# Optimization experiments

Hardware: AMD Instinct MI355X
Metric: run time of the kernel (lower is better)

The kernel has to match this reference:

```python
import jax, jax.numpy as jnp
import numpy as np
import math

DIM_EMB = 1024
DIM_QK = 1024
DIM_V = 1024
NORM_FACT = 1.0 / math.sqrt(DIM_EMB)

def setup_inputs() -> dict:
    key = jax.random.key(0)
    k0, k1, k2, k3 = jax.random.split(key, 4)
    x = jax.random.normal(k0, (4, 4096, DIM_EMB), dtype=jnp.float32)
    # nn.Linear weights are [out_features, in_features]; y = x @ W.T
    s = 1.0 / math.sqrt(DIM_EMB)
    Wq = jax.random.uniform(k1, (DIM_QK, DIM_EMB), jnp.float32, -s, s)
    Wk = jax.random.uniform(k2, (DIM_QK, DIM_EMB), jnp.float32, -s, s)
    Wv = jax.random.uniform(k3, (DIM_V, DIM_EMB), jnp.float32, -s, s)
    return {"x": x, "Wq": Wq, "Wk": Wk, "Wv": Wv}

def reference(x, Wq, Wk, Wv):
    # q,k,v: [b, n, d]
    q = jnp.einsum('bne,de->bnd', x, Wq)
    k = jnp.einsum('bne,de->bnd', x, Wk)
    v = jnp.einsum('bne,de->bnd', x, Wv)
    logits = jnp.einsum('bnd,bmd->bnm', q, k)  # [b, n, n]
    # Faithful to source: softmax over last dim FIRST, then scale by 1/sqrt(dim_embedding)
    score = jax.nn.softmax(logits, axis=-1) * NORM_FACT
    att = jnp.einsum('bnm,bmv->bnv', score, v)
    return att
```

## Files before the change

### kernel.cpp

```cpp
#include <hip/hip_runtime.h>
#include <hip/hip_bf16.h>

typedef _Float16 f16;
typedef _Float16 f16x4 __attribute__((ext_vector_type(4)));
typedef _Float16 f16x8 __attribute__((ext_vector_type(8)));
typedef float f32x4 __attribute__((ext_vector_type(4)));

__device__ __forceinline__ void gload16(const void* g, void* l) {
    __builtin_amdgcn_global_load_lds(
        (const __attribute__((address_space(1))) void*)g,
        (__attribute__((address_space(3))) void*)l, 16, 0, 0);
}

#define FENCE asm volatile("" ::: "memory")
#define BARRIER do { FENCE; __builtin_amdgcn_s_barrier(); FENCE; } while (0)

#define PHASE_MFMA(QI, QJ)                                                    \
    __builtin_amdgcn_s_setprio(1);                                            \
    _Pragma("unroll")                                                         \
    for (int ks = 0; ks < 2; ++ks)                                            \
      _Pragma("unroll")                                                       \
      for (int i = 0; i < 4; ++i)                                             \
        _Pragma("unroll")                                                     \
        for (int j = 0; j < 2; ++j)                                           \
          acc[(QI)*4 + i][(QJ)*2 + j] = __builtin_amdgcn_mfma_f32_16x16x32_f16( \
              a[i][ks], b[j][ks], acc[(QI)*4 + i][(QJ)*2 + j], 0, 0, 0);      \
    __builtin_amdgcn_s_setprio(0);

#define BT8_BODY(KBASE, NTILES)                                               \
    const int rr8 = lane >> 3;                                                \
    const int cs  = ((lane & 7) ^ rr8) << 3;                                  \
    const int ldsr = wid << 3;                                                \
    auto stageA = [&](int kt, int c, int h) {                                 \
        const size_t g0 = (size_t)(bm + (h << 7) + ldsr + rr8) * lda + (KBASE) + kt + cs; \
        gload16(A + g0,                      &sA[c][((h << 7) + ldsr) << 6]); \
        gload16(A + g0 + ((size_t)lda << 6), &sA[c][((h << 7) + 64 + ldsr) << 6]); \
    };                                                                        \
    auto stageB = [&](int kt, int c, int h) {                                 \
        const size_t g0 = (size_t)(bn + (h << 7) + ldsr + rr8) * ldb + (KBASE) + kt + cs; \
        gload16(B + g0,                      &sB[c][((h << 7) + ldsr) << 6]); \
        gload16(B + g0 + ((size_t)ldb << 6), &sB[c][((h << 7) + 64 + ldsr) << 6]); \
    };                                                                        \
    f32x4 acc[8][4] = {};                                                     \
    f16x8 a[4][2], b[2][2];                                                   \
    auto loadA = [&](int c, int qi) {                                         \
        _Pragma("unroll")                                                     \
        for (int i = 0; i < 4; ++i) {                                         \
            const int ra = wr * 128 + (qi * 4 + i) * 16 + (lane & 15);        \
            const int swz = (ra & 7) << 3;                                    \
            _Pragma("unroll")                                                 \
            for (int ks = 0; ks < 2; ++ks) {                                  \
                const int kk = ks * 32 + (lane >> 4) * 8;                     \
                a[i][ks] = *(const f16x8*)(&sA[c][(ra << 6) + (kk ^ swz)]);   \
            }                                                                 \
        }                                                                     \
    };                                                                        \
    auto loadB = [&](int c, int qj) {                                         \
        _Pragma("unroll")                                                     \
        for (int j = 0; j < 2; ++j) {                                         \
            const int rb = wc * 64 + (qj * 2 + j) * 16 + (lane & 15);         \
            const int swz = (rb & 7) << 3;                                    \
            _Pragma("unroll")                                                 \
            for (int ks = 0; ks < 2; ++ks) {                                  \
                const int kk = ks * 32 + (lane >> 4) * 8;                     \
                b[j][ks] = *(const f16x8*)(&sB[c][(rb << 6) + (kk ^ swz)]);   \
            }                                                                 \
        }                                                                     \
    };                                                                        \
    stageA(0, 0, 0); stageA(0, 0, 1); stageB(0, 0, 0); stageB(0, 0, 1);       \
    asm volatile("s_waitcnt vmcnt(0)" ::: "memory");                          \
    BARRIER;                                                                  \
    for (int g = 0; g < (NTILES); ++g) {                                      \
        const int c = g & 1, cn = c ^ 1;                                      \
        const int kn = (g + 1) << 6;                                          \
        const bool more = (g + 1) < (NTILES);                                 \
        loadA(c, 0); loadB(c, 0);                                             \
        if (more) { stageA(kn, cn, 0); stageA(kn, cn, 1); }                   \
        BARRIER; PHASE_MFMA(0, 0); BARRIER;                                   \
        loadB(c, 1);                                                          \
        if (more) { stageB(kn, cn, 0); stageB(kn, cn, 1); }                   \
        BARRIER; PHASE_MFMA(0, 1); BARRIER;                                   \
        loadA(c, 1); loadB(c, 0);                                             \
        BARRIER; PHASE_MFMA(1, 0); BARRIER;                                   \
        loadB(c, 1);                                                          \
        asm volatile("s_waitcnt vmcnt(0)" ::: "memory");                      \
        BARRIER; PHASE_MFMA(1, 1); BARRIER;                                   \
    }

template<bool F16OUT>
__global__ __launch_bounds__(512) void gemm_bt8(
    const f16* __restrict__ A, const f16* __restrict__ B, void* __restrict__ Cv,
    int K, int lda, int ldb, int ldc, float scale, int nbn)
{
    __shared__ f16 sA[2][256 * 64];
    __shared__ f16 sB[2][256 * 64];
    const int tid = threadIdx.x, lane = tid & 63, wid = tid >> 6;
    const int wr = wid >> 2, wc = wid & 3;
    const int cpx = gridDim.x >> 3;
    const int wg = (blockIdx.x & 7) * cpx + (blockIdx.x >> 3);
    const int bm = (wg / nbn) << 8, bn = (wg % nbn) << 8;

    BT8_BODY(0, K >> 6)

#pragma unroll
    for (int i = 0; i < 8; ++i)
#pragma unroll
        for (int j = 0; j < 4; ++j)
#pragma unroll
            for (int r = 0; r < 4; ++r) {
                const int row = bm + wr * 128 + i * 16 + ((lane >> 4) << 2) + r;
                const int col = bn + wc * 64 + j * 16 + (lane & 15);
                if constexpr (F16OUT)
                    ((f16*)Cv)[(size_t)row * ldc + col] = (f16)(acc[i][j][r] * scale);
                else
                    ((float*)Cv)[(size_t)row * ldc + col] = acc[i][j][r] * scale;
            }
}

__global__ __launch_bounds__(512) void gemm_qk(
    const f16* __restrict__ A, const f16* __restrict__ B,
    f16* __restrict__ P, float* __restrict__ mst, float* __restrict__ sst,
    int lda, int ldb)
{
    __shared__ f16 sA[2][256 * 64];
    __shared__ f16 sB[2][256 * 64];
    const int tid = threadIdx.x, lane = tid & 63, wid = tid >> 6;
    const int wr = wid >> 2, wc = wid & 3;
    const int cpx = gridDim.x >> 3;
    const int wg = (blockIdx.x & 7) * cpx + (blockIdx.x >> 3);
    const int bm = (wg >> 4) << 8, bn = (wg & 15) << 8;

    BT8_BODY(0, 16)

    float* red = (float*)sA;
    const int lg = lane >> 4;
#pragma unroll
    for (int i = 0; i < 8; ++i)
#pragma unroll
        for (int r = 0; r < 4; ++r) {
            float v = fmaxf(fmaxf(acc[i][0][r], acc[i][1][r]),
                            fmaxf(acc[i][2][r], acc[i][3][r]));
#pragma unroll
            for (int msk = 1; msk <= 8; msk <<= 1) v = fmaxf(v, __shfl_xor(v, msk));
            if ((lane & 15) == 0) red[wr * 512 + (i * 16 + lg * 4 + r) * 4 + wc] = v;
        }
    BARRIER;
    float mloc[8][4];
#pragma unroll
    for (int i = 0; i < 8; ++i)
#pragma unroll
        for (int r = 0; r < 4; ++r) {
            const float4 q = *(const float4*)&red[wr * 512 + (i * 16 + lg * 4 + r) * 4];
            mloc[i][r] = fmaxf(fmaxf(q.x, q.y), fmaxf(q.z, q.w));
        }
    BARRIER;
#pragma unroll
    for (int i = 0; i < 8; ++i)
#pragma unroll
        for (int r = 0; r < 4; ++r) {
            float s = 0.f;
#pragma unroll
            for (int j = 0; j < 4; ++j) {
                const float e = __expf(acc[i][j][r] - mloc[i][r]);
                acc[i][j][r] = e; s += e;
            }
#pragma unroll
            for (int msk = 1; msk <= 8; msk <<= 1) s += __shfl_xor(s, msk);
            if ((lane & 15) == 0) red[wr * 512 + (i * 16 + lg * 4 + r) * 4 + wc] = s;
        }
    BARRIER;
    const int t4 = bn >> 8;
    if ((lane & 15) == 0) {
#pragma unroll
        for (int i = 0; i < 8; ++i)
#pragma unroll
            for (int r = 0; r < 4; ++r) {
                const int row128 = i * 16 + lg * 4 + r;
                const float4 q = *(const float4*)&red[wr * 512 + row128 * 4];
                const int grow = bm + wr * 128 + row128;
                mst[t4 * 4096 + grow] = mloc[i][r];
                sst[t4 * 4096 + grow] = (q.x + q.y) + (q.z + q.w);
            }
    }
#pragma unroll
    for (int i = 0; i < 8; ++i)
#pragma unroll
        for (int j = 0; j < 4; ++j)
#pragma unroll
            for (int r = 0; r < 4; ++r) {
                const int grow = bm + wr * 128 + i * 16 + lg * 4 + r;
                const int gcol = bn + wc * 64 + j * 16 + (lane & 15);
                P[(size_t)grow * 4096 + gcol] = (f16)acc[i][j][r];
            }
}

__global__ __launch_bounds__(256) void scale_p(
    f16* __restrict__ P, const float* __restrict__ mst, const float* __restrict__ sst)
{
    const int row = blockIdx.x;
    float m = -1e30f;
#pragma unroll
    for (int t = 0; t < 16; ++t) m = fmaxf(m, mst[t * 4096 + row]);
    float l = 0.f;
#pragma unroll
    for (int t = 0; t < 16; ++t) l += sst[t * 4096 + row] * __expf(mst[t * 4096 + row] - m);
    const float inv = 1.0f / (32.0f * l);
    const float f = __expf(mst[(threadIdx.x >> 4) * 4096 + row] - m) * inv;
    f16* p = P + (size_t)row * 4096 + threadIdx.x * 16;
    f16x8 va = *(f16x8*)p, vb = *(f16x8*)(p + 8);
#pragma unroll
    for (int u = 0; u < 8; ++u) {
        va[u] = (f16)((float)va[u] * f);
        vb[u] = (f16)((float)vb[u] * f);
    }
    *(f16x8*)p = va;
    *(f16x8*)(p + 8) = vb;
}

__global__ __launch_bounds__(512) void gemm_pv8(
    const f16* __restrict__ A, const f16* __restrict__ B, float* __restrict__ Cout,
    f16* __restrict__ Pp, int lda, int ldb)
{
    __shared__ f16 sA[2][256 * 64];
    __shared__ f16 sB[2][256 * 64];
    const int tid = threadIdx.x, lane = tid & 63, wid = tid >> 6;
    const int wr = wid >> 2, wc = wid & 3;
    const int cpx = gridDim.x >> 3;
    const int wg = (blockIdx.x & 7) * cpx + (blockIdx.x >> 3);
    const int bm = (wg >> 2) << 8, bn = (wg & 3) << 8;
    const int z = blockIdx.y;
    const int kbase = z << 10;

    BT8_BODY(kbase, 16)

#pragma unroll
    for (int i = 0; i < 8; ++i)
#pragma unroll
        for (int j = 0; j < 4; ++j)
#pragma unroll
            for (int r = 0; r < 4; ++r) {
                const int row = bm + wr * 128 + i * 16 + ((lane >> 4) << 2) + r;
                const int col = bn + wc * 64 + j * 16 + (lane & 15);
                const float v = acc[i][j][r];
                if (z == 3)
                    Cout[((size_t)row << 10) + col] = v;
                else
                    Pp[(size_t)z * 4194304 + ((size_t)row << 10) + col] = (f16)v;
            }
}

__global__ __launch_bounds__(256) void reduce_pv(
    float* __restrict__ Cout, const f16* __restrict__ Pp)
{
    const int i = blockIdx.x * 256 + threadIdx.x;
    const int r = i >> 7;
    const int c = (i & 127) << 3;
    const size_t base = ((size_t)r << 10) + c;
    const f16x8 p0 = *(const f16x8*)(Pp + base);
    const f16x8 p1 = *(const f16x8*)(Pp + base + 4194304);
    const f16x8 p2 = *(const f16x8*)(Pp + base + 8388608);
    float* o = Cout + base;
    float4 o0 = *(float4*)o, o1 = *(float4*)(o + 4);
    o0.x += (float)p0[0] + (float)p1[0] + (float)p2[0];
    o0.y += (float)p0[1] + (float)p1[1] + (float)p2[1];
    o0.z += (float)p0[2] + (float)p1[2] + (float)p2[2];
    o0.w += (float)p0[3] + (float)p1[3] + (float)p2[3];
    o1.x += (float)p0[4] + (float)p1[4] + (float)p2[4];
    o1.y += (float)p0[5] + (float)p1[5] + (float)p2[5];
    o1.z += (float)p0[6] + (float)p1[6] + (float)p2[6];
    o1.w += (float)p0[7] + (float)p1[7] + (float)p2[7];
    *(float4*)o = o0;
    *(float4*)(o + 4) = o1;
}

template<bool F16IN, bool F16OUT, bool PIPE>
__global__ __launch_bounds__(256) void gemm_bt(
    const void* __restrict__ Av, const void* __restrict__ Bv, void* __restrict__ Cv,
    int K, int lda, int ldb, int ldc, float scale)
{
    constexpr int NB = PIPE ? 2 : 1;
    __shared__ f16 sA[NB][128 * 64];
    __shared__ f16 sB[NB][128 * 64];
    const int tid = threadIdx.x, lane = tid & 63, wid = tid >> 6;
    const int wr = wid >> 1, wc = wid & 1;
    const int bm = blockIdx.x * 128, bn = blockIdx.y * 128;

    f32x4 acc[4][4] = {};

    auto stage16 = [&](int kt, int bsel) {
        const f16* A = (const f16*)Av;
        const f16* B = (const f16*)Bv;
        const int rsub = lane >> 3;
        const int csw = ((lane & 7) ^ rsub) << 3;
#pragma unroll
        for (int i = 0; i < 4; ++i) {
            const int rb = (wid * 4 + i) * 8;
            gload16(A + (size_t)(bm + rb + rsub) * lda + kt + csw, &sA[bsel][rb * 64]);
            gload16(B + (size_t)(bn + rb + rsub) * ldb + kt + csw, &sB[bsel][rb * 64]);
        }
    };

    auto compute = [&](int bsel) {
#pragma unroll
        for (int ks = 0; ks < 2; ++ks) {
            const int kk = ks * 32 + (lane >> 4) * 8;
            f16x8 a[4], b[4];
#pragma unroll
            for (int i = 0; i < 4; ++i) {
                const int ra = wr * 64 + i * 16 + (lane & 15);
                a[i] = *(const f16x8*)(&sA[bsel][(ra << 6) + (kk ^ ((ra & 7) << 3))]);
                const int rb2 = wc * 64 + i * 16 + (lane & 15);
                b[i] = *(const f16x8*)(&sB[bsel][(rb2 << 6) + (kk ^ ((rb2 & 7) << 3))]);
            }
#pragma unroll
            for (int i = 0; i < 4; ++i)
#pragma unroll
                for (int j = 0; j < 4; ++j)
                    acc[i][j] = __builtin_amdgcn_mfma_f32_16x16x32_f16(a[i], b[j], acc[i][j], 0, 0, 0);
        }
    };

    if constexpr (PIPE) {
        stage16(0, 0);
        asm volatile("s_waitcnt vmcnt(0)" ::: "memory");
        __syncthreads();
        const int NT2 = K >> 6;
        for (int t = 0; t < NT2; ++t) {
            if (t + 1 < NT2) stage16((t + 1) << 6, (t + 1) & 1);
            compute(t & 1);
            asm volatile("s_waitcnt vmcnt(0)" ::: "memory");
            __builtin_amdgcn_s_barrier();
        }
    } else {
        for (int kt = 0; kt < K; kt += 64) {
            __syncthreads();
            stage16(kt, 0);
            __syncthreads();
            compute(0);
        }
    }
#pragma unroll
    for (int i = 0; i < 4; ++i)
#pragma unroll
        for (int j = 0; j < 4; ++j)
#pragma unroll
            for (int r = 0; r < 4; ++r) {
                const int row = bm + wr * 64 + i * 16 + (lane >> 4) * 4 + r;
                const int col = bn + wc * 64 + j * 16 + (lane & 15);
                if constexpr (F16OUT)
                    ((f16*)Cv)[(size_t)row * ldc + col] = (f16)acc[i][j][r];
                else
                    ((float*)Cv)[(size_t)row * ldc + col] = acc[i][j][r] * scale;
            }
}

__global__ __launch_bounds__(256) void cvt_f16(
    const float* __restrict__ s, f16* __restrict__ d, int n8)
{
    int i = blockIdx.x * 256 + threadIdx.x;
    const int stride = gridDim.x * 256;
    for (; i < n8; i += stride) {
        const float4 a = ((const float4*)s)[i * 2];
        const float4 b = ((const float4*)s)[i * 2 + 1];
        f16x8 o = { (f16)a.x, (f16)a.y, (f16)a.z, (f16)a.w,
                    (f16)b.x, (f16)b.y, (f16)b.z, (f16)b.w };
        ((f16x8*)d)[i] = o;
    }
}

extern "C" void kernel_launch(void* const* d_in, const int* in_sizes, int n_in,
                              void* d_out, int out_size, void* d_ws, size_t ws_size,
                              hipStream_t stream) {
    const float* x  = (const float*)d_in[0];
    const float* Wq = (const float*)d_in[1];
    const float* Wk = (const float*)d_in[2];
    const float* Wv = (const float*)d_in[3];
    float* out = (float*)d_out;

    f16*   qk  = (f16*)d_out;
    f16*   xh  = (f16*)d_ws;
    f16*   wqh = xh + 16384LL * 1024;
    f16*   wkh = wqh + 1024LL * 1024;

    f16*   P   = (f16*)d_ws;
    float* mst = (float*)((char*)d_ws + (32LL << 20));
    float* sst = mst + 16 * 4096;
    f16*   Pp  = (f16*)((char*)d_ws + (32LL << 20));
    f16*   vTw = (f16*)((char*)d_ws + (56LL << 20));

    cvt_f16<<<1024, 256, 0, stream>>>(x,  xh,  16384 * 1024 / 8);
    cvt_f16<<<512,  256, 0, stream>>>(Wq, wqh, 1024 * 1024 / 8);
    cvt_f16<<<512,  256, 0, stream>>>(Wk, wkh, 1024 * 1024 / 8);

    gemm_bt8<true><<<256, 512, 0, stream>>>(xh, wqh, qk,        1024, 1024, 1024, 2048, 1.f, 4);
    gemm_bt8<true><<<256, 512, 0, stream>>>(xh, wkh, qk + 1024, 1024, 1024, 1024, 2048, 1.f, 4);

    for (int b = 0; b < 4; ++b) {
        const size_t tb = (size_t)b * 4096;
        f16* xhb = (f16*)(out + tb * 1024);
        f16* wvh = xhb + 4096LL * 1024;
        gemm_qk<<<256, 512, 0, stream>>>(
            qk + tb * 2048, qk + tb * 2048 + 1024, P, mst, sst, 2048, 2048);
        scale_p<<<4096, 256, 0, stream>>>(P, mst, sst);
        cvt_f16<<<1024, 256, 0, stream>>>(x + tb * 1024, xhb, 4096 * 1024 / 8);
        cvt_f16<<<512,  256, 0, stream>>>(Wv, wvh, 1024 * 1024 / 8);
        gemm_bt<true, true, true><<<dim3(8, 32), 256, 0, stream>>>(
            wvh, xhb, vTw, 1024, 1024, 1024, 4096, 1.f);
        gemm_pv8<<<dim3(64, 4), 512, 0, stream>>>(
            P, vTw, out + tb * 1024, Pp, 4096, 4096);
        reduce_pv<<<2048, 256, 0, stream>>>(out + tb * 1024, Pp);
    }
}
```

Measured before the change: 706.5 us.

## Store raw logits coalesced via LDS and do full-row softmax in separate pass

gemm_qk now skips the in-block partial softmax with its cross-wave reductions and barriers. It transposes the accumulators through swizzled LDS so the f16 logits go out as coalesced 16-byte stores instead of scattered 2-byte stores. A new softmax_f16 kernel computes each row's max, sum and normalisation in one wave, replacing the max/sum statistics and the rescale pass. The separate fp32-to-f16 conversion launches are also merged into single kernels. Storing raw logits in f16 instead of exponentials may reduce accuracy.

```diff
diff --git a/kernel.cpp b/kernel.cpp
--- a/kernel.cpp
+++ b/kernel.cpp
@@ -119,8 +119,7 @@
 
 __global__ __launch_bounds__(512) void gemm_qk(
     const f16* __restrict__ A, const f16* __restrict__ B,
-    f16* __restrict__ P, float* __restrict__ mst, float* __restrict__ sst,
-    int lda, int ldb)
+    f16* __restrict__ S, int lda, int ldb)
 {
     __shared__ f16 sA[2][256 * 64];
     __shared__ f16 sB[2][256 * 64];
@@ -132,89 +131,67 @@
 
     BT8_BODY(0, 16)
 
-    float* red = (float*)sA;
-    const int lg = lane >> 4;
-#pragma unroll
-    for (int i = 0; i < 8; ++i)
-#pragma unroll
-        for (int r = 0; r < 4; ++r) {
-            float v = fmaxf(fmaxf(acc[i][0][r], acc[i][1][r]),
-                            fmaxf(acc[i][2][r], acc[i][3][r]));
-#pragma unroll
-            for (int msk = 1; msk <= 8; msk <<= 1) v = fmaxf(v, __shfl_xor(v, msk));
-            if ((lane & 15) == 0) red[wr * 512 + (i * 16 + lg * 4 + r) * 4 + wc] = v;
+    {
+        f16* Tb = wr ? (f16*)sB : (f16*)sA;
+        const int lg = lane >> 4;
+#pragma unroll
+        for (int i = 0; i < 8; ++i)
+#pragma unroll
+            for (int j = 0; j < 4; ++j)
+#pragma unroll
+                for (int r = 0; r < 4; ++r) {
+                    const int rloc = i * 16 + lg * 4 + r;
+                    const int col  = wc * 64 + j * 16 + (lane & 15);
+                    Tb[rloc * 256 + (col ^ (((rloc >> 2) & 7) << 3))] = (f16)acc[i][j][r];
+                }
+    }
+    BARRIER;
+#pragma unroll
+    for (int u = 0; u < 16; ++u) {
+        const int gi = u * 512 + tid;
+        const int row = gi >> 5;
+        const int c0 = (gi & 31) << 3;
+        const f16* Tb = (row & 128) ? (const f16*)sB : (const f16*)sA;
+        f16x8 v = *(const f16x8*)(Tb + (row & 127) * 256
+                                  + (c0 ^ (((row >> 2) & 7) << 3)));
+        *(f16x8*)(S + (size_t)(bm + row) * 4096 + bn + c0) = v;
+    }
+}
+
+__global__ __launch_bounds__(256) void softmax_f16(f16* S)
+{
+    const int lane = threadIdx.x & 63, wid = threadIdx.x >> 6;
+    const int row = blockIdx.x * 4 + wid;
+    f16* src = S + (size_t)row * 4096;
+    f16x8 v[8];
+#pragma unroll
+    for (int u = 0; u < 8; ++u) v[u] = *(const f16x8*)(src + u * 512 + lane * 8);
+    float m = -1e30f;
+#pragma unroll
+    for (int u = 0; u < 8; ++u)
+#pragma unroll
+        for (int e = 0; e < 8; ++e) m = fmaxf(m, (float)v[u][e]);
+#pragma unroll
+    for (int msk = 1; msk <= 32; msk <<= 1) m = fmaxf(m, __shfl_xor(m, msk));
+    float ev[64];
+    float s = 0.f;
+#pragma unroll
+    for (int u = 0; u < 8; ++u)
+#pragma unroll
+        for (int e = 0; e < 8; ++e) {
+            const float x = __expf((float)v[u][e] - m);
+            ev[u * 8 + e] = x; s += x;
         }
-    BARRIER;
-    float mloc[8][4];
-#pragma unroll
-    for (int i = 0; i < 8; ++i)
-#pragma unroll
-        for (int r = 0; r < 4; ++r) {
-            const float4 q = *(const float4*)&red[wr * 512 + (i * 16 + lg * 4 + r) * 4];
-            mloc[i][r] = fmaxf(fmaxf(q.x, q.y), fmaxf(q.z, q.w));
-        }
-    BARRIER;
-#pragma unroll
-    for (int i = 0; i < 8; ++i)
-#pragma unroll
-        for (int r = 0; r < 4; ++r) {
-            float s = 0.f;
-#pragma unroll
-            for (int j = 0; j < 4; ++j) {
-                const float e = __expf(acc[i][j][r] - mloc[i][r]);
-                acc[i][j][r] = e; s += e;
-            }
-#pragma unroll
-            for (int msk = 1; msk <= 8; msk <<= 1) s += __shfl_xor(s, msk);
-            if ((lane & 15) == 0) red[wr * 512 + (i * 16 + lg * 4 + r) * 4 + wc] = s;
-        }
-    BARRIER;
-    const int t4 = bn >> 8;
-    if ((lane & 15) == 0) {
-#pragma unroll
-        for (int i = 0; i < 8; ++i)
-#pragma unroll
-            for (int r = 0; r < 4; ++r) {
-                const int row128 = i * 16 + lg * 4 + r;
-                const float4 q = *(const float4*)&red[wr * 512 + row128 * 4];
-                const int grow = bm + wr * 128 + row128;
-                mst[t4 * 4096 + grow] = mloc[i][r];
-                sst[t4 * 4096 + grow] = (q.x + q.y) + (q.z + q.w);
-            }
-    }
-#pragma unroll
-    for (int i = 0; i < 8; ++i)
-#pragma unroll
-        for (int j = 0; j < 4; ++j)
-#pragma unroll
-            for (int r = 0; r < 4; ++r) {
-                const int grow = bm + wr * 128 + i * 16 + lg * 4 + r;
-                const int gcol = bn + wc * 64 + j * 16 + (lane & 15);
-                P[(size_t)grow * 4096 + gcol] = (f16)acc[i][j][r];
-            }
-}
-
-__global__ __launch_bounds__(256) void scale_p(
-    f16* __restrict__ P, const float* __restrict__ mst, const float* __restrict__ sst)
-{
-    const int row = blockIdx.x;
-    float m = -1e30f;
-#pragma unroll
-    for (int t = 0; t < 16; ++t) m = fmaxf(m, mst[t * 4096 + row]);
-    float l = 0.f;
-#pragma unroll
-    for (int t = 0; t < 16; ++t) l += sst[t * 4096 + row] * __expf(mst[t * 4096 + row] - m);
-    const float inv = 1.0f / (32.0f * l);
-    const float f = __expf(mst[(threadIdx.x >> 4) * 4096 + row] - m) * inv;
-    f16* p = P + (size_t)row * 4096 + threadIdx.x * 16;
-    f16x8 va = *(f16x8*)p, vb = *(f16x8*)(p + 8);
+#pragma unroll
+    for (int msk = 1; msk <= 32; msk <<= 1) s += __shfl_xor(s, msk);
+    const float inv = 1.0f / (32.0f * s);
 #pragma unroll
     for (int u = 0; u < 8; ++u) {
-        va[u] = (f16)((float)va[u] * f);
-        vb[u] = (f16)((float)vb[u] * f);
-    }
-    *(f16x8*)p = va;
-    *(f16x8*)(p + 8) = vb;
+        f16x8 p;
+#pragma unroll
+        for (int e = 0; e < 8; ++e) p[e] = (f16)(ev[u * 8 + e] * inv);
+        *(f16x8*)(src + u * 512 + lane * 8) = p;
+    }
 }
 
 __global__ __launch_bounds__(512) void gemm_pv8(
@@ -273,14 +250,12 @@
     *(float4*)(o + 4) = o1;
 }
 
-template<bool F16IN, bool F16OUT, bool PIPE>
-__global__ __launch_bounds__(256) void gemm_bt(
-    const void* __restrict__ Av, const void* __restrict__ Bv, void* __restrict__ Cv,
-    int K, int lda, int ldb, int ldc, float scale)
-{
-    constexpr int NB = PIPE ? 2 : 1;
-    __shared__ f16 sA[NB][128 * 64];
-    __shared__ f16 sB[NB][128 * 64];
+__global__ __launch_bounds__(256) void gemm_vt(
+    const f16* __restrict__ A, const f16* __restrict__ B, f16* __restrict__ C,
+    int K, int lda, int ldb, int ldc)
+{
+    __shared__ f16 sA[2][128 * 64];
+    __shared__ f16 sB[2][128 * 64];
     const int tid = threadIdx.x, lane = tid & 63, wid = tid >> 6;
     const int wr = wid >> 1, wc = wid & 1;
     const int bm = blockIdx.x * 128, bn = blockIdx.y * 128;
@@ -288,8 +263,6 @@
     f32x4 acc[4][4] = {};
 
     auto stage16 = [&](int kt, int bsel) {
-        const f16* A = (const f16*)Av;
-        const f16* B = (const f16*)Bv;
         const int rsub = lane >> 3;
         const int csw = ((lane & 7) ^ rsub) << 3;
 #pragma unroll
@@ -320,24 +293,15 @@
         }
     };
 
-    if constexpr (PIPE) {
-        stage16(0, 0);
+    stage16(0, 0);
+    asm volatile("s_waitcnt vmcnt(0)" ::: "memory");
+    __syncthreads();
+    const int NT2 = K >> 6;
+    for (int t = 0; t < NT2; ++t) {
+        if (t + 1 < NT2) stage16((t + 1) << 6, (t + 1) & 1);
+        compute(t & 1);
         asm volatile("s_waitcnt vmcnt(0)" ::: "memory");
-        __syncthreads();
-        const int NT2 = K >> 6;
-        for (int t = 0; t < NT2; ++t) {
-            if (t + 1 < NT2) stage16((t + 1) << 6, (t + 1) & 1);
-            compute(t & 1);
-            asm volatile("s_waitcnt vmcnt(0)" ::: "memory");
-            __builtin_amdgcn_s_barrier();
-        }
-    } else {
-        for (int kt = 0; kt < K; kt += 64) {
-            __syncthreads();
-            stage16(kt, 0);
-            __syncthreads();
-            compute(0);
-        }
+        __builtin_amdgcn_s_barrier();
     }
 #pragma unroll
     for (int i = 0; i < 4; ++i)
@@ -347,25 +311,39 @@
             for (int r = 0; r < 4; ++r) {
                 const int row = bm + wr * 64 + i * 16 + (lane >> 4) * 4 + r;
                 const int col = bn + wc * 64 + j * 16 + (lane & 15);
-                if constexpr (F16OUT)
-                    ((f16*)Cv)[(size_t)row * ldc + col] = (f16)acc[i][j][r];
-                else
-                    ((float*)Cv)[(size_t)row * ldc + col] = acc[i][j][r] * scale;
+                C[(size_t)row * ldc + col] = (f16)acc[i][j][r];
             }
 }
 
-__global__ __launch_bounds__(256) void cvt_f16(
-    const float* __restrict__ s, f16* __restrict__ d, int n8)
-{
-    int i = blockIdx.x * 256 + threadIdx.x;
-    const int stride = gridDim.x * 256;
-    for (; i < n8; i += stride) {
-        const float4 a = ((const float4*)s)[i * 2];
-        const float4 b = ((const float4*)s)[i * 2 + 1];
-        f16x8 o = { (f16)a.x, (f16)a.y, (f16)a.z, (f16)a.w,
-                    (f16)b.x, (f16)b.y, (f16)b.z, (f16)b.w };
-        ((f16x8*)d)[i] = o;
-    }
+__global__ __launch_bounds__(256) void cvt3(
+    const float* __restrict__ x, const float* __restrict__ wq, const float* __restrict__ wk,
+    f16* __restrict__ dx, f16* __restrict__ dwq, f16* __restrict__ dwk)
+{
+    const int i = blockIdx.x * 256 + threadIdx.x;
+    const float* s; f16* d; int off;
+    if (i < 2097152)      { s = x;  d = dx;  off = i; }
+    else if (i < 2228224) { s = wq; d = dwq; off = i - 2097152; }
+    else                  { s = wk; d = dwk; off = i - 2228224; }
+    const float4 a = ((const float4*)s)[off * 2];
+    const float4 b = ((const float4*)s)[off * 2 + 1];
+    f16x8 o = { (f16)a.x, (f16)a.y, (f16)a.z, (f16)a.w,
+                (f16)b.x, (f16)b.y, (f16)b.z, (f16)b.w };
+    ((f16x8*)d)[off] = o;
+}
+
+__global__ __launch_bounds__(256) void cvt_batch(
+    const float* __restrict__ xb, const float* __restrict__ wv,
+    f16* __restrict__ dxb, f16* __restrict__ dwv)
+{
+    const int i = blockIdx.x * 256 + threadIdx.x;
+    const float* s; f16* d; int off;
+    if (i < 524288) { s = xb; d = dxb; off = i; }
+    else            { s = wv; d = dwv; off = i - 524288; }
+    const float4 a = ((const float4*)s)[off * 2];
+    const float4 b = ((const float4*)s)[off * 2 + 1];
+    f16x8 o = { (f16)a.x, (f16)a.y, (f16)a.z, (f16)a.w,
+                (f16)b.x, (f16)b.y, (f16)b.z, (f16)b.w };
+    ((f16x8*)d)[off] = o;
 }
 
 extern "C" void kernel_launch(void* const* d_in, const int* in_sizes, int n_in,
@@ -379,18 +357,14 @@
 
     f16*   qk  = (f16*)d_out;
     f16*   xh  = (f16*)d_ws;
-    f16*   wqh = xh + 16384LL * 1024;
+    f16*   wqh = (f16*)((char*)d_ws + (32LL << 20));
     f16*   wkh = wqh + 1024LL * 1024;
 
-    f16*   P   = (f16*)d_ws;
-    float* mst = (float*)((char*)d_ws + (32LL << 20));
-    float* sst = mst + 16 * 4096;
+    f16*   S   = (f16*)d_ws;
     f16*   Pp  = (f16*)((char*)d_ws + (32LL << 20));
     f16*   vTw = (f16*)((char*)d_ws + (56LL << 20));
 
-    cvt_f16<<<1024, 256, 0, stream>>>(x,  xh,  16384 * 1024 / 8);
-    cvt_f16<<<512,  256, 0, stream>>>(Wq, wqh, 1024 * 1024 / 8);
-    cvt_f16<<<512,  256, 0, stream>>>(Wk, wkh, 1024 * 1024 / 8);
+    cvt3<<<9216, 256, 0, stream>>>(x, Wq, Wk, xh, wqh, wkh);
 
     gemm_bt8<true><<<256, 512, 0, stream>>>(xh, wqh, qk,        1024, 1024, 1024, 2048, 1.f, 4);
     gemm_bt8<true><<<256, 512, 0, stream>>>(xh, wkh, qk + 1024, 1024, 1024, 1024, 2048, 1.f, 4);
@@ -400,14 +374,11 @@
         f16* xhb = (f16*)(out + tb * 1024);
         f16* wvh = xhb + 4096LL * 1024;
         gemm_qk<<<256, 512, 0, stream>>>(
-            qk + tb * 2048, qk + tb * 2048 + 1024, P, mst, sst, 2048, 2048);
-        scale_p<<<4096, 256, 0, stream>>>(P, mst, sst);
-        cvt_f16<<<1024, 256, 0, stream>>>(x + tb * 1024, xhb, 4096 * 1024 / 8);
-        cvt_f16<<<512,  256, 0, stream>>>(Wv, wvh, 1024 * 1024 / 8);
-        gemm_bt<true, true, true><<<dim3(8, 32), 256, 0, stream>>>(
-            wvh, xhb, vTw, 1024, 1024, 1024, 4096, 1.f);
-        gemm_pv8<<<dim3(64, 4), 512, 0, stream>>>(
-            P, vTw, out + tb * 1024, Pp, 4096, 4096);
+            qk + tb * 2048, qk + tb * 2048 + 1024, S, 2048, 2048);
+        softmax_f16<<<1024, 256, 0, stream>>>(S);
+        cvt_batch<<<2560, 256, 0, stream>>>(x + tb * 1024, Wv, xhb, wvh);
+        gemm_vt<<<dim3(8, 32), 256, 0, stream>>>(wvh, xhb, vTw, 1024, 1024, 1024, 4096);
+        gemm_pv8<<<dim3(64, 4), 512, 0, stream>>>(S, vTw, out + tb * 1024, Pp, 4096, 4096);
         reduce_pv<<<2048, 256, 0, stream>>>(out + tb * 1024, Pp);
     }
 }
```

Result: faster. 565.5 us (-20.0%).
